# Kernel tuning notes

Measured on AMD Instinct MI355X. Metric: run time of the kernel, lower is better.

Reference implementation:

```python
import jax, jax.numpy as jnp
import numpy as np

W_BIT = 8

def quantize_weight(w, k=W_BIT):
    # DoReFa-style weight quantization (conv2d_Q_fn): tanh-normalize to [0,1],
    # uniform-quantize to 2^k-1 levels (round with straight-through), map to [-1,1].
    n = float(2 ** k - 1)
    t = jnp.tanh(w)
    t = t / (2.0 * jnp.max(jnp.abs(t))) + 0.5
    q = t + jax.lax.stop_gradient(jnp.round(t * n) / n - t)
    return 2.0 * q - 1.0

def qconv(x, w, b, pad):
    wq = quantize_weight(w)
    y = jax.lax.conv_general_dilated(
        x, wq, window_strides=(1, 1), padding=[(pad, pad), (pad, pad)],
        dimension_numbers=('NCHW', 'OIHW', 'NCHW'))
    return y + b[None, :, None, None]

def upsample2x(x):
    # nearest-neighbor, scale_factor=2
    return jnp.repeat(jnp.repeat(x, 2, axis=2), 2, axis=3)

def setup_inputs() -> dict:
    key = jax.random.key(0)
    ks = jax.random.split(key, 11)
    F = 256
    C3 = jax.random.normal(ks[0], (8, 512, 64, 64), dtype=jnp.float32)
    C4 = jax.random.normal(ks[1], (8, 1024, 32, 32), dtype=jnp.float32)
    C5 = jax.random.normal(ks[2], (8, 2048, 16, 16), dtype=jnp.float32)
    # conv params (torch nn.Conv2d default has bias)
    w5 = jax.random.normal(ks[3], (F, 2048, 1, 1), dtype=jnp.float32) * 0.02
    b5 = jax.random.normal(ks[4], (F,), dtype=jnp.float32) * 0.01
    w4 = jax.random.normal(ks[5], (F, 1024, 1, 1), dtype=jnp.float32) * 0.02
    b4 = jax.random.normal(ks[6], (F,), dtype=jnp.float32) * 0.01
    w3 = jax.random.normal(ks[7], (F, 512, 1, 1), dtype=jnp.float32) * 0.02
    b3 = jax.random.normal(ks[8], (F,), dtype=jnp.float32) * 0.01
    w3_2 = jax.random.normal(ks[9], (F, F, 3, 3), dtype=jnp.float32) * 0.02
    b3_2 = jax.random.normal(ks[10], (F,), dtype=jnp.float32) * 0.01
    return {"C3": C3, "C4": C4, "C5": C5,
            "w5": w5, "b5": b5, "w4": w4, "b4": b4,
            "w3": w3, "b3": b3, "w3_2": w3_2, "b3_2": b3_2}

def reference(C3, C4, C5, w5, b5, w4, b4, w3, b3, w3_2, b3_2):
    P5_x = qconv(C5, w5, b5, pad=0)            # [B,256,16,16]
    P5_up = upsample2x(P5_x)                   # [B,256,32,32]
    P4_x = qconv(C4, w4, b4, pad=0) + P5_up    # [B,256,32,32]
    P4_up = upsample2x(P4_x)                   # [B,256,64,64]
    P3_x = qconv(C3, w3, b3, pad=0) + P4_up    # [B,256,64,64]
    P3_x = qconv(P3_x, w3_2, b3_2, pad=1)      # [B,256,64,64]
    return P3_x
```

## Files before the change

kernel.cpp:

```cpp
#include <hip/hip_runtime.h>
#include <stdint.h>

typedef unsigned short u16;
typedef short s16x8 __attribute__((ext_vector_type(8)));
typedef short s16x4 __attribute__((ext_vector_type(4)));
typedef float f32x4 __attribute__((ext_vector_type(4)));
typedef unsigned int u32x4 __attribute__((ext_vector_type(4)));

__device__ __forceinline__ u16 f2bf(float x) {
    unsigned u = __float_as_uint(x);
    unsigned r = u + 0x7FFFu + ((u >> 16) & 1u);
    return (u16)(r >> 16);
}

__device__ __forceinline__ void gll16(void* lds, const void* g) {
    __builtin_amdgcn_global_load_lds(
        (const __attribute__((address_space(1))) void*)g,
        (__attribute__((address_space(3))) void*)lds,
        16, 0, 0);
}

__global__ __launch_bounds__(256) void reduce_maxabs(
    const float* __restrict__ a0, int n0, const float* __restrict__ a1, int n1,
    const float* __restrict__ a2, int n2, const float* __restrict__ a3, int n3,
    float* __restrict__ out) {
    int which = blockIdx.y;
    const float* w = which == 0 ? a0 : which == 1 ? a1 : which == 2 ? a2 : a3;
    int n = which == 0 ? n0 : which == 1 ? n1 : which == 2 ? n2 : n3;
    float m = 0.f;
    for (int i = blockIdx.x * 256 + threadIdx.x; i < n; i += gridDim.x * 256)
        m = fmaxf(m, fabsf(tanhf(w[i])));
#pragma unroll
    for (int off = 32; off > 0; off >>= 1)
        m = fmaxf(m, __shfl_down(m, off, 64));
    __shared__ float sm[4];
    if ((threadIdx.x & 63) == 0) sm[threadIdx.x >> 6] = m;
    __syncthreads();
    if (threadIdx.x == 0) {
        m = fmaxf(fmaxf(sm[0], sm[1]), fmaxf(sm[2], sm[3]));
        atomicMax((int*)out + which, __float_as_int(m));
    }
}

__global__ __launch_bounds__(256) void prep(
    const float* __restrict__ w5, const float* __restrict__ w4,
    const float* __restrict__ w3, const float* __restrict__ w32,
    const float* __restrict__ mx,
    u16* __restrict__ q5, u16* __restrict__ q4,
    u16* __restrict__ q3, u16* __restrict__ q2,
    const float* __restrict__ C5, const float* __restrict__ C4,
    const float* __restrict__ C3,
    u16* __restrict__ c5n, u16* __restrict__ c4n, u16* __restrict__ c3n) {
    __shared__ float tile[64][65];
    int t = threadIdx.x;
    int b = blockIdx.x;
    if (b < 5888) {
        int which, i;
        const float* w;
        if (b < 2048)      { which = 0; w = w5;  i = b * 256 + t; }
        else if (b < 3072) { which = 1; w = w4;  i = (b - 2048) * 256 + t; }
        else if (b < 3584) { which = 2; w = w3;  i = (b - 3072) * 256 + t; }
        else               { which = 3; w = w32; i = (b - 3584) * 256 + t; }
        float inv = 0.5f / mx[which];
        float tt = tanhf(w[i]) * inv + 0.5f;
        float q = rintf(tt * 255.f) * (1.f / 255.f);
        u16 o = f2bf(2.f * q - 1.f);
        if (which == 0) q5[i] = o;
        else if (which == 1) q4[i] = o;
        else if (which == 2) q3[i] = o;
        else {
            int kw = i % 3, kh = (i / 3) % 3, c = (i / 9) & 255, f = i / 2304;
            q2[(size_t)((kh * 3 + kw) * 256 + f) * 256 + c] = o;
        }
        return;
    }
    b -= 5888;
    const float* src; u16* dst; int C, HW, bx, by, nn;
    if (b < 1024) {
        nn = b >> 7; int r = b & 127; by = r >> 2; bx = r & 3;
        C = 2048; HW = 256; src = C5; dst = c5n;
    } else if (b < 3072) {
        int l = b - 1024; nn = l >> 8; int r = l & 255; by = r >> 4; bx = r & 15;
        C = 1024; HW = 1024; src = C4; dst = c4n;
    } else {
        int l = b - 3072; nn = l >> 9; int r = l & 511; by = r >> 6; bx = r & 63;
        C = 512; HW = 4096; src = C3; dst = c3n;
    }
    int hw0 = bx << 6, c0 = by << 6;
    const float* s2 = src + (size_t)nn * C * HW;
#pragma unroll
    for (int j = 0; j < 4; ++j) {
        int c = (t >> 4) + j * 16;
        int hw = (t & 15) << 2;
        f32x4 v = *(const f32x4*)(s2 + (size_t)(c0 + c) * HW + hw0 + hw);
        tile[c][hw] = v.x; tile[c][hw + 1] = v.y; tile[c][hw + 2] = v.z; tile[c][hw + 3] = v.w;
    }
    __syncthreads();
    u16* d2 = dst + (size_t)nn * C * HW;
#pragma unroll
    for (int j = 0; j < 4; ++j) {
        int idx = j * 256 + t;
        int c4 = (idx & 15) << 2, hw = idx >> 4;
        s16x4 o;
        o.x = (short)f2bf(tile[c4][hw]);
        o.y = (short)f2bf(tile[c4 + 1][hw]);
        o.z = (short)f2bf(tile[c4 + 2][hw]);
        o.w = (short)f2bf(tile[c4 + 3][hw]);
        *(s16x4*)(d2 + (size_t)(hw0 + hw) * C + c0 + c4) = o;
    }
}

template<int BF, int BPX, int FJ, int FI>
__global__ __launch_bounds__(256) void gemm_qconv(
    const u16* __restrict__ A, const u16* __restrict__ B,
    const float* __restrict__ bias, const float* __restrict__ addsrc,
    float* __restrict__ outF, u16* __restrict__ outB,
    int Kfull, int Kchunk, int Wlog, int HWlog, int atomic_out) {
    __shared__ u16 As[BF * 64];
    __shared__ u16 Bs[BPX * 64];
    int t = threadIdx.x, lane = t & 63, wv = t >> 6;
    int l16 = lane & 15, quad = lane >> 4;
    int f0 = blockIdx.y * BF, p0 = blockIdx.x * BPX;
    int wf = (wv >> 1) * (BF / 2), wp = (wv & 1) * (BPX / 2);
    f32x4 acc[FJ][FI] = {};
    const u16* Ab = A + (size_t)f0 * Kfull;
    const u16* Bb = B + (size_t)p0 * Kfull;
    int row = t >> 3, c8 = t & 7;
    int k_begin = blockIdx.z * Kchunk, k_end = k_begin + Kchunk;
    for (int k0 = k_begin; k0 < k_end; k0 += 64) {
#pragma unroll
        for (int it = 0; it < BF / 32; ++it)
            gll16(&As[(it * 256 + wv * 64) * 8], Ab + (size_t)(it * 32 + row) * Kfull + k0 + c8 * 8);
#pragma unroll
        for (int it = 0; it < BPX / 32; ++it)
            gll16(&Bs[(it * 256 + wv * 64) * 8], Bb + (size_t)(it * 32 + row) * Kfull + k0 + c8 * 8);
        __syncthreads();
#pragma unroll
        for (int kk = 0; kk < 64; kk += 32) {
            s16x8 a[FJ], b[FI];
#pragma unroll
            for (int j = 0; j < FJ; ++j)
                a[j] = *(const s16x8*)&As[(wf + 16 * j + l16) * 64 + kk + quad * 8];
#pragma unroll
            for (int i = 0; i < FI; ++i)
                b[i] = *(const s16x8*)&Bs[(wp + 16 * i + l16) * 64 + kk + quad * 8];
#pragma unroll
            for (int j = 0; j < FJ; ++j)
#pragma unroll
                for (int i = 0; i < FI; ++i)
                    acc[j][i] = __builtin_amdgcn_mfma_f32_16x16x32_bf16(a[j], b[i], acc[j][i], 0, 0, 0);
        }
        __syncthreads();
    }
    int W = 1 << Wlog;
    bool bias_on = (blockIdx.z == 0);
#pragma unroll
    for (int j = 0; j < FJ; ++j) {
        int f = f0 + wf + 16 * j + (quad << 2);
        f32x4 bz = {0.f, 0.f, 0.f, 0.f};
        if (bias_on) bz = *(const f32x4*)(bias + f);
#pragma unroll
        for (int i = 0; i < FI; ++i) {
            int px = p0 + wp + 16 * i + l16;
            f32x4 v = acc[j][i] + bz;
            if (addsrc) {
                int n = px >> HWlog;
                int rem = px & ((1 << HWlog) - 1);
                int h = rem >> Wlog, ww = rem & (W - 1);
                int sp = (n << (HWlog - 2)) + ((h >> 1) << (Wlog - 1)) + (ww >> 1);
                v += *(const f32x4*)(addsrc + (size_t)sp * 256 + f);
            }
            if (atomic_out) {
                float* d = outF + (size_t)px * 256 + f;
                atomicAdd(d + 0, v.x); atomicAdd(d + 1, v.y);
                atomicAdd(d + 2, v.z); atomicAdd(d + 3, v.w);
            } else if (outB) {
                s16x4 o;
                o.x = (short)f2bf(v.x); o.y = (short)f2bf(v.y);
                o.z = (short)f2bf(v.z); o.w = (short)f2bf(v.w);
                *(s16x4*)(outB + (size_t)px * 256 + f) = o;
            } else {
                *(f32x4*)(outF + (size_t)px * 256 + f) = v;
            }
        }
    }
}

#define CVS 40
__global__ __launch_bounds__(256) void conv3x3_q(
    const u16* __restrict__ X, const u16* __restrict__ Wq,
    const float* __restrict__ bias, float* __restrict__ outp) {
    __shared__ u16 Rg[6 * 66 * CVS];
    __shared__ u16 Aw[5 * 64 * CVS];
    int t = threadIdx.x, lane = t & 63, wv = t >> 6;
    int l16 = lane & 15, quad = lane >> 4;
    int n = blockIdx.x >> 4, h0 = (blockIdx.x & 15) << 2;
    int f0 = blockIdx.y << 6;
    f32x4 acc[4][4] = {};
    for (int c0 = 0; c0 < 256; c0 += 32) {
#pragma unroll
        for (int it = 0; it < 7; ++it) {
            int chunk = it * 256 + t;
            if (chunk < 1584) {
                int r = chunk / 264;
                int rest = chunk - r * 264;
                int w = rest >> 2, c8 = rest & 3;
                int h = h0 - 1 + r, ww = w - 1;
                u32x4 v; v.x = 0; v.y = 0; v.z = 0; v.w = 0;
                if ((unsigned)h < 64u && (unsigned)ww < 64u)
                    v = *(const u32x4*)(X + ((((size_t)n << 12) + (h << 6) + ww) << 8) + c0 + c8 * 8);
                *(u32x4*)(Rg + (r * 66 + w) * CVS + c8 * 8) = v;
            }
        }
#pragma unroll
        for (int it = 0; it < 5; ++it) {
            int chunk = it * 256 + t;
            int tap = chunk >> 8, fr = (chunk >> 2) & 63, cc = chunk & 3;
            *(u32x4*)(Aw + (tap * 64 + fr) * CVS + cc * 8) =
                *(const u32x4*)(Wq + (((size_t)tap * 256 + f0 + fr) << 8) + c0 + cc * 8);
        }
        __syncthreads();
#pragma unroll
        for (int tp = 0; tp < 5; ++tp) {
            int dh = tp / 3, dw = tp % 3;
            s16x8 a[4], b[4];
#pragma unroll
            for (int i = 0; i < 4; ++i)
                b[i] = *(const s16x8*)(Rg + ((wv + dh) * 66 + 16 * i + l16 + dw) * CVS + quad * 8);
#pragma unroll
            for (int j = 0; j < 4; ++j)
                a[j] = *(const s16x8*)(Aw + (tp * 64 + 16 * j + l16) * CVS + quad * 8);
#pragma unroll
            for (int j = 0; j < 4; ++j)
#pragma unroll
                for (int i = 0; i < 4; ++i)
                    acc[j][i] = __builtin_amdgcn_mfma_f32_16x16x32_bf16(a[j], b[i], acc[j][i], 0, 0, 0);
        }
        __syncthreads();
#pragma unroll
        for (int it = 0; it < 4; ++it) {
            int chunk = it * 256 + t;
            int tap = 5 + (chunk >> 8), fr = (chunk >> 2) & 63, cc = chunk & 3;
            *(u32x4*)(Aw + ((tap - 5) * 64 + fr) * CVS + cc * 8) =
                *(const u32x4*)(Wq + (((size_t)tap * 256 + f0 + fr) << 8) + c0 + cc * 8);
        }
        __syncthreads();
#pragma unroll
        for (int tp = 5; tp < 9; ++tp) {
            int dh = tp / 3, dw = tp % 3;
            s16x8 a[4], b[4];
#pragma unroll
            for (int i = 0; i < 4; ++i)
                b[i] = *(const s16x8*)(Rg + ((wv + dh) * 66 + 16 * i + l16 + dw) * CVS + quad * 8);
#pragma unroll
            for (int j = 0; j < 4; ++j)
                a[j] = *(const s16x8*)(Aw + ((tp - 5) * 64 + 16 * j + l16) * CVS + quad * 8);
#pragma unroll
            for (int j = 0; j < 4; ++j)
#pragma unroll
                for (int i = 0; i < 4; ++i)
                    acc[j][i] = __builtin_amdgcn_mfma_f32_16x16x32_bf16(a[j], b[i], acc[j][i], 0, 0, 0);
        }
        __syncthreads();
    }
    int h = h0 + wv;
#pragma unroll
    for (int j = 0; j < 4; ++j) {
        int f = f0 + 16 * j + (quad << 2);
        f32x4 bz = *(const f32x4*)(bias + f);
#pragma unroll
        for (int i = 0; i < 4; ++i) {
            int w = 16 * i + l16;
#pragma unroll
            for (int r = 0; r < 4; ++r)
                outp[((size_t)(n * 256 + f + r) << 12) + (h << 6) + w] = acc[j][i][r] + bz[r];
        }
    }
}

extern "C" void kernel_launch(void* const* d_in, const int* in_sizes, int n_in,
                              void* d_out, int out_size, void* d_ws, size_t ws_size,
                              hipStream_t stream) {
    (void)in_sizes; (void)n_in; (void)out_size; (void)ws_size;
    const float* C3  = (const float*)d_in[0];
    const float* C4  = (const float*)d_in[1];
    const float* C5  = (const float*)d_in[2];
    const float* w5  = (const float*)d_in[3];
    const float* b5  = (const float*)d_in[4];
    const float* w4  = (const float*)d_in[5];
    const float* b4  = (const float*)d_in[6];
    const float* w3  = (const float*)d_in[7];
    const float* b3  = (const float*)d_in[8];
    const float* w32 = (const float*)d_in[9];
    const float* b32 = (const float*)d_in[10];
    float* outp = (float*)d_out;

    char* p = (char*)d_ws;
    float* mx = (float*)p;  p += 256;
    u16* q5   = (u16*)p;    p += (size_t)524288 * 2;
    u16* q4   = (u16*)p;    p += (size_t)262144 * 2;
    u16* q3   = (u16*)p;    p += (size_t)131072 * 2;
    u16* q2   = (u16*)p;    p += (size_t)589824 * 2;
    u16* c5n  = (u16*)p;    p += (size_t)4194304 * 2;
    u16* c4n  = (u16*)p;    p += (size_t)8388608 * 2;
    u16* c3n  = (u16*)p;    p += (size_t)16777216 * 2;
    float* p5x = (float*)p; p += (size_t)2097152 * 4;
    float* p4x = (float*)p; p += (size_t)8388608 * 4;
    u16* p3xn = (u16*)p;    p += (size_t)8388608 * 2;

    hipMemsetAsync(mx, 0, 256, stream);
    hipMemsetAsync(p5x, 0, (size_t)2097152 * 4, stream);
    reduce_maxabs<<<dim3(128, 4), 256, 0, stream>>>(w5, 524288, w4, 262144,
                                                    w3, 131072, w32, 589824, mx);
    prep<<<13056, 256, 0, stream>>>(w5, w4, w3, w32, mx, q5, q4, q3, q2,
                                    C5, C4, C3, c5n, c4n, c3n);
    gemm_qconv<64, 64, 2, 2><<<dim3(32, 4, 2), 256, 0, stream>>>(
        q5, c5n, b5, nullptr, p5x, nullptr, 2048, 1024, 4, 8, 1);
    gemm_qconv<64, 128, 2, 4><<<dim3(64, 4, 1), 256, 0, stream>>>(
        q4, c4n, b4, p5x, p4x, nullptr, 1024, 1024, 5, 10, 0);
    gemm_qconv<128, 128, 4, 4><<<dim3(256, 2, 1), 256, 0, stream>>>(
        q3, c3n, b3, p4x, nullptr, p3xn, 512, 512, 6, 12, 0);
    conv3x3_q<<<dim3(128, 4), 256, 0, stream>>>(p3xn, q2, b32, outp);
}
```

Measured before the change: 305.6 us.

## Split prep kernel, widen transpose, bf16 P4 intermediate, direct-load conv3x3 weights

Several changes land together. The max-abs reduction now takes max|w| and applies tanh once afterwards, which is valid because tanh is monotonic. Prep is split into a weight-quantization kernel and a transpose kernel using 128-channel tiles with 16-byte bf16 stores. The P4 intermediate is stored as bf16 instead of fp32 to halve its traffic, and the P5 GEMM uses split-K of 4. The conv3x3 kernel drops its LDS staging of weights and reads weight fragments straight from global memory, which removes barriers but risks uncoalesced or repeated global reads. Storing P4 in bf16 also adds some rounding error to the P4-to-P3 path.

```diff
diff --git a/kernel.cpp b/kernel.cpp
--- a/kernel.cpp
+++ b/kernel.cpp
@@ -11,6 +11,9 @@
     unsigned u = __float_as_uint(x);
     unsigned r = u + 0x7FFFu + ((u >> 16) & 1u);
     return (u16)(r >> 16);
+}
+__device__ __forceinline__ float bf2f(u16 h) {
+    return __uint_as_float((unsigned)h << 16);
 }
 
 __device__ __forceinline__ void gll16(void* lds, const void* g) {
@@ -29,7 +32,7 @@
     int n = which == 0 ? n0 : which == 1 ? n1 : which == 2 ? n2 : n3;
     float m = 0.f;
     for (int i = blockIdx.x * 256 + threadIdx.x; i < n; i += gridDim.x * 256)
-        m = fmaxf(m, fabsf(tanhf(w[i])));
+        m = fmaxf(m, fabsf(w[i]));
 #pragma unroll
     for (int off = 32; off > 0; off >>= 1)
         m = fmaxf(m, __shfl_down(m, off, 64));
@@ -42,55 +45,50 @@
     }
 }
 
-__global__ __launch_bounds__(256) void prep(
+__global__ __launch_bounds__(256) void quant_w(
     const float* __restrict__ w5, const float* __restrict__ w4,
     const float* __restrict__ w3, const float* __restrict__ w32,
     const float* __restrict__ mx,
     u16* __restrict__ q5, u16* __restrict__ q4,
-    u16* __restrict__ q3, u16* __restrict__ q2,
+    u16* __restrict__ q3, u16* __restrict__ q2) {
+    int b = blockIdx.x, t = threadIdx.x;
+    int which, i;
+    const float* w;
+    if (b < 2048)      { which = 0; w = w5;  i = b * 256 + t; }
+    else if (b < 3072) { which = 1; w = w4;  i = (b - 2048) * 256 + t; }
+    else if (b < 3584) { which = 2; w = w3;  i = (b - 3072) * 256 + t; }
+    else               { which = 3; w = w32; i = (b - 3584) * 256 + t; }
+    float inv = 0.5f / tanhf(mx[which]);
+    float tt = tanhf(w[i]) * inv + 0.5f;
+    float q = rintf(tt * 255.f) * (1.f / 255.f);
+    u16 o = f2bf(2.f * q - 1.f);
+    if (which == 0) q5[i] = o;
+    else if (which == 1) q4[i] = o;
+    else if (which == 2) q3[i] = o;
+    else {
+        int kw = i % 3, kh = (i / 3) % 3, c = (i / 9) & 255, f = i / 2304;
+        q2[(size_t)((kh * 3 + kw) * 256 + f) * 256 + c] = o;
+    }
+}
+
+__global__ __launch_bounds__(256) void transpose_nhwc(
     const float* __restrict__ C5, const float* __restrict__ C4,
     const float* __restrict__ C3,
     u16* __restrict__ c5n, u16* __restrict__ c4n, u16* __restrict__ c3n) {
-    __shared__ float tile[64][65];
-    int t = threadIdx.x;
-    int b = blockIdx.x;
-    if (b < 5888) {
-        int which, i;
-        const float* w;
-        if (b < 2048)      { which = 0; w = w5;  i = b * 256 + t; }
-        else if (b < 3072) { which = 1; w = w4;  i = (b - 2048) * 256 + t; }
-        else if (b < 3584) { which = 2; w = w3;  i = (b - 3072) * 256 + t; }
-        else               { which = 3; w = w32; i = (b - 3584) * 256 + t; }
-        float inv = 0.5f / mx[which];
-        float tt = tanhf(w[i]) * inv + 0.5f;
-        float q = rintf(tt * 255.f) * (1.f / 255.f);
-        u16 o = f2bf(2.f * q - 1.f);
-        if (which == 0) q5[i] = o;
-        else if (which == 1) q4[i] = o;
-        else if (which == 2) q3[i] = o;
-        else {
-            int kw = i % 3, kh = (i / 3) % 3, c = (i / 9) & 255, f = i / 2304;
-            q2[(size_t)((kh * 3 + kw) * 256 + f) * 256 + c] = o;
-        }
-        return;
-    }
-    b -= 5888;
-    const float* src; u16* dst; int C, HW, bx, by, nn;
-    if (b < 1024) {
-        nn = b >> 7; int r = b & 127; by = r >> 2; bx = r & 3;
-        C = 2048; HW = 256; src = C5; dst = c5n;
-    } else if (b < 3072) {
-        int l = b - 1024; nn = l >> 8; int r = l & 255; by = r >> 4; bx = r & 15;
-        C = 1024; HW = 1024; src = C4; dst = c4n;
-    } else {
-        int l = b - 3072; nn = l >> 9; int r = l & 511; by = r >> 6; bx = r & 63;
-        C = 512; HW = 4096; src = C3; dst = c3n;
-    }
-    int hw0 = bx << 6, c0 = by << 6;
+    __shared__ float tile[128][65];
+    int t = threadIdx.x, b = blockIdx.x;
+    const float* src; u16* dst; int C, HW, cb, hwb, nn;
+    if (b < 512)       { nn = b >> 6; int r = b & 63; cb = r >> 2; hwb = r & 3;
+                         C = 2048; HW = 256;  src = C5; dst = c5n; }
+    else if (b < 1536) { int l = b - 512;  nn = l >> 7; int r = l & 127; cb = r >> 4; hwb = r & 15;
+                         C = 1024; HW = 1024; src = C4; dst = c4n; }
+    else               { int l = b - 1536; nn = l >> 8; int r = l & 255; cb = r >> 6; hwb = r & 63;
+                         C = 512;  HW = 4096; src = C3; dst = c3n; }
+    int c0 = cb << 7, hw0 = hwb << 6;
     const float* s2 = src + (size_t)nn * C * HW;
 #pragma unroll
-    for (int j = 0; j < 4; ++j) {
-        int c = (t >> 4) + j * 16;
+    for (int i = 0; i < 8; ++i) {
+        int c = (t >> 4) + (i << 4);
         int hw = (t & 15) << 2;
         f32x4 v = *(const f32x4*)(s2 + (size_t)(c0 + c) * HW + hw0 + hw);
         tile[c][hw] = v.x; tile[c][hw + 1] = v.y; tile[c][hw + 2] = v.z; tile[c][hw + 3] = v.w;
@@ -98,24 +96,23 @@
     __syncthreads();
     u16* d2 = dst + (size_t)nn * C * HW;
 #pragma unroll
-    for (int j = 0; j < 4; ++j) {
-        int idx = j * 256 + t;
-        int c4 = (idx & 15) << 2, hw = idx >> 4;
-        s16x4 o;
-        o.x = (short)f2bf(tile[c4][hw]);
-        o.y = (short)f2bf(tile[c4 + 1][hw]);
-        o.z = (short)f2bf(tile[c4 + 2][hw]);
-        o.w = (short)f2bf(tile[c4 + 3][hw]);
-        *(s16x4*)(d2 + (size_t)(hw0 + hw) * C + c0 + c4) = o;
-    }
-}
-
-template<int BF, int BPX, int FJ, int FI>
+    for (int i = 0; i < 4; ++i) {
+        int hw = (t >> 4) + (i << 4);
+        int g = t & 15;
+        s16x8 o;
+#pragma unroll
+        for (int j = 0; j < 8; ++j) o[j] = (short)f2bf(tile[8 * g + j][hw]);
+        *(s16x8*)(d2 + (size_t)(hw0 + hw) * C + c0 + 8 * g) = o;
+    }
+}
+
+template<int BF, int BPX, int FJ, int FI, int ATOMIC>
 __global__ __launch_bounds__(256) void gemm_qconv(
     const u16* __restrict__ A, const u16* __restrict__ B,
-    const float* __restrict__ bias, const float* __restrict__ addsrc,
+    const float* __restrict__ bias,
+    const float* __restrict__ addF, const u16* __restrict__ addB,
     float* __restrict__ outF, u16* __restrict__ outB,
-    int Kfull, int Kchunk, int Wlog, int HWlog, int atomic_out) {
+    int Kfull, int Kchunk, int Wlog, int HWlog) {
     __shared__ u16 As[BF * 64];
     __shared__ u16 Bs[BPX * 64];
     int t = threadIdx.x, lane = t & 63, wv = t >> 6;
@@ -163,24 +160,31 @@
         for (int i = 0; i < FI; ++i) {
             int px = p0 + wp + 16 * i + l16;
             f32x4 v = acc[j][i] + bz;
-            if (addsrc) {
-                int n = px >> HWlog;
-                int rem = px & ((1 << HWlog) - 1);
-                int h = rem >> Wlog, ww = rem & (W - 1);
-                int sp = (n << (HWlog - 2)) + ((h >> 1) << (Wlog - 1)) + (ww >> 1);
-                v += *(const f32x4*)(addsrc + (size_t)sp * 256 + f);
-            }
-            if (atomic_out) {
+            if (ATOMIC) {
                 float* d = outF + (size_t)px * 256 + f;
                 atomicAdd(d + 0, v.x); atomicAdd(d + 1, v.y);
                 atomicAdd(d + 2, v.z); atomicAdd(d + 3, v.w);
-            } else if (outB) {
-                s16x4 o;
-                o.x = (short)f2bf(v.x); o.y = (short)f2bf(v.y);
-                o.z = (short)f2bf(v.z); o.w = (short)f2bf(v.w);
-                *(s16x4*)(outB + (size_t)px * 256 + f) = o;
             } else {
-                *(f32x4*)(outF + (size_t)px * 256 + f) = v;
+                if (addF || addB) {
+                    int n = px >> HWlog;
+                    int rem = px & ((1 << HWlog) - 1);
+                    int h = rem >> Wlog, ww = rem & (W - 1);
+                    int sp = (n << (HWlog - 2)) + ((h >> 1) << (Wlog - 1)) + (ww >> 1);
+                    if (addF) v += *(const f32x4*)(addF + (size_t)sp * 256 + f);
+                    else {
+                        s16x4 av = *(const s16x4*)(addB + (size_t)sp * 256 + f);
+                        v.x += bf2f((u16)av.x); v.y += bf2f((u16)av.y);
+                        v.z += bf2f((u16)av.z); v.w += bf2f((u16)av.w);
+                    }
+                }
+                if (outB) {
+                    s16x4 o;
+                    o.x = (short)f2bf(v.x); o.y = (short)f2bf(v.y);
+                    o.z = (short)f2bf(v.z); o.w = (short)f2bf(v.w);
+                    *(s16x4*)(outB + (size_t)px * 256 + f) = o;
+                } else {
+                    *(f32x4*)(outF + (size_t)px * 256 + f) = v;
+                }
             }
         }
     }
@@ -191,7 +195,6 @@
     const u16* __restrict__ X, const u16* __restrict__ Wq,
     const float* __restrict__ bias, float* __restrict__ outp) {
     __shared__ u16 Rg[6 * 66 * CVS];
-    __shared__ u16 Aw[5 * 64 * CVS];
     int t = threadIdx.x, lane = t & 63, wv = t >> 6;
     int l16 = lane & 15, quad = lane >> 4;
     int n = blockIdx.x >> 4, h0 = (blockIdx.x & 15) << 2;
@@ -212,16 +215,9 @@
                 *(u32x4*)(Rg + (r * 66 + w) * CVS + c8 * 8) = v;
             }
         }
-#pragma unroll
-        for (int it = 0; it < 5; ++it) {
-            int chunk = it * 256 + t;
-            int tap = chunk >> 8, fr = (chunk >> 2) & 63, cc = chunk & 3;
-            *(u32x4*)(Aw + (tap * 64 + fr) * CVS + cc * 8) =
-                *(const u32x4*)(Wq + (((size_t)tap * 256 + f0 + fr) << 8) + c0 + cc * 8);
-        }
-        __syncthreads();
-#pragma unroll
-        for (int tp = 0; tp < 5; ++tp) {
+        __syncthreads();
+#pragma unroll
+        for (int tp = 0; tp < 9; ++tp) {
             int dh = tp / 3, dw = tp % 3;
             s16x8 a[4], b[4];
 #pragma unroll
@@ -229,32 +225,7 @@
                 b[i] = *(const s16x8*)(Rg + ((wv + dh) * 66 + 16 * i + l16 + dw) * CVS + quad * 8);
 #pragma unroll
             for (int j = 0; j < 4; ++j)
-                a[j] = *(const s16x8*)(Aw + (tp * 64 + 16 * j + l16) * CVS + quad * 8);
-#pragma unroll
-            for (int j = 0; j < 4; ++j)
-#pragma unroll
-                for (int i = 0; i < 4; ++i)
-                    acc[j][i] = __builtin_amdgcn_mfma_f32_16x16x32_bf16(a[j], b[i], acc[j][i], 0, 0, 0);
-        }
-        __syncthreads();
-#pragma unroll
-        for (int it = 0; it < 4; ++it) {
-            int chunk = it * 256 + t;
-            int tap = 5 + (chunk >> 8), fr = (chunk >> 2) & 63, cc = chunk & 3;
-            *(u32x4*)(Aw + ((tap - 5) * 64 + fr) * CVS + cc * 8) =
-                *(const u32x4*)(Wq + (((size_t)tap * 256 + f0 + fr) << 8) + c0 + cc * 8);
-        }
-        __syncthreads();
-#pragma unroll
-        for (int tp = 5; tp < 9; ++tp) {
-            int dh = tp / 3, dw = tp % 3;
-            s16x8 a[4], b[4];
-#pragma unroll
-            for (int i = 0; i < 4; ++i)
-                b[i] = *(const s16x8*)(Rg + ((wv + dh) * 66 + 16 * i + l16 + dw) * CVS + quad * 8);
-#pragma unroll
-            for (int j = 0; j < 4; ++j)
-                a[j] = *(const s16x8*)(Aw + ((tp - 5) * 64 + 16 * j + l16) * CVS + quad * 8);
+                a[j] = *(const s16x8*)(Wq + (((size_t)tp * 256 + f0 + 16 * j + l16) << 8) + c0 + quad * 8);
 #pragma unroll
             for (int j = 0; j < 4; ++j)
 #pragma unroll
@@ -305,20 +276,20 @@
     u16* c4n  = (u16*)p;    p += (size_t)8388608 * 2;
     u16* c3n  = (u16*)p;    p += (size_t)16777216 * 2;
     float* p5x = (float*)p; p += (size_t)2097152 * 4;
-    float* p4x = (float*)p; p += (size_t)8388608 * 4;
+    u16* p4x  = (u16*)p;    p += (size_t)8388608 * 2;
     u16* p3xn = (u16*)p;    p += (size_t)8388608 * 2;
 
     hipMemsetAsync(mx, 0, 256, stream);
     hipMemsetAsync(p5x, 0, (size_t)2097152 * 4, stream);
     reduce_maxabs<<<dim3(128, 4), 256, 0, stream>>>(w5, 524288, w4, 262144,
                                                     w3, 131072, w32, 589824, mx);
-    prep<<<13056, 256, 0, stream>>>(w5, w4, w3, w32, mx, q5, q4, q3, q2,
-                                    C5, C4, C3, c5n, c4n, c3n);
-    gemm_qconv<64, 64, 2, 2><<<dim3(32, 4, 2), 256, 0, stream>>>(
-        q5, c5n, b5, nullptr, p5x, nullptr, 2048, 1024, 4, 8, 1);
-    gemm_qconv<64, 128, 2, 4><<<dim3(64, 4, 1), 256, 0, stream>>>(
-        q4, c4n, b4, p5x, p4x, nullptr, 1024, 1024, 5, 10, 0);
-    gemm_qconv<128, 128, 4, 4><<<dim3(256, 2, 1), 256, 0, stream>>>(
-        q3, c3n, b3, p4x, nullptr, p3xn, 512, 512, 6, 12, 0);
+    quant_w<<<5888, 256, 0, stream>>>(w5, w4, w3, w32, mx, q5, q4, q3, q2);
+    transpose_nhwc<<<3584, 256, 0, stream>>>(C5, C4, C3, c5n, c4n, c3n);
+    gemm_qconv<64, 64, 2, 2, 1><<<dim3(32, 4, 4), 256, 0, stream>>>(
+        q5, c5n, b5, nullptr, nullptr, p5x, nullptr, 2048, 512, 4, 8);
+    gemm_qconv<64, 128, 2, 4, 0><<<dim3(64, 4, 1), 256, 0, stream>>>(
+        q4, c4n, b4, p5x, nullptr, nullptr, p4x, 1024, 1024, 5, 10);
+    gemm_qconv<128, 128, 4, 4, 0><<<dim3(256, 2, 1), 256, 0, stream>>>(
+        q3, c3n, b3, nullptr, p4x, nullptr, p3xn, 512, 512, 6, 12);
     conv3x3_q<<<dim3(128, 4), 256, 0, stream>>>(p3xn, q2, b32, outp);
 }
```

Measured after the change: 351.0 us. 1.15x slower.
